# Kernel tuning notes

Measured on AMD Instinct MI355X. Metric: run time of the kernel, lower is better.

The kernel has to match this reference:

```python
import jax, jax.numpy as jnp
import numpy as np


def setup_inputs() -> dict:
    key = jax.random.key(0)
    k1, k2, k3, k4 = jax.random.split(key, 4)
    B, T, M, Din, Dout = 32, 24, 512, 64, 64
    x = jax.random.normal(k1, (B, T, M, Din), dtype=jnp.float32)
    adj = jax.random.uniform(k2, (M, M), dtype=jnp.float32)
    adj = adj / jnp.sum(adj, axis=-1, keepdims=True)  # row-normalized adjacency
    route_weights = jax.random.normal(k3, (M, Din, Dout), dtype=jnp.float32) * 0.05
    route_bias = jax.random.normal(k4, (M, 1, Dout), dtype=jnp.float32) * 0.05
    return {"x": x, "adj": adj, "route_weights": route_weights, "route_bias": route_bias}


def reference(x, adj, route_weights, route_bias):
    B, T, M, _ = x.shape
    xf = x.reshape(B * T, M, -1)                      # [BT, M, Din]
    # shared adjacency applied across all B*T graphs: one contraction instead of
    # a broadcast bmm
    h = jnp.einsum('mn,bnd->bmd', adj, xf)            # [BT, M, Din]
    # per-node (per-route) weight transform + per-route bias
    h = jnp.einsum('bmd,mdl->bml', h, route_weights)  # [BT, M, Dout]
    h = h + route_bias[:, 0, :][None, :, :]           # bias per route m
    return h.reshape(B, T, M, -1)
```

## Files before the change

### kernel.cpp

```cpp
#include <hip/hip_runtime.h>
#include <stdint.h>

typedef short bf16x8 __attribute__((ext_vector_type(8)));
typedef unsigned short u16x8 __attribute__((ext_vector_type(8)));
typedef float f32x4 __attribute__((ext_vector_type(4)));
typedef float f32x8 __attribute__((ext_vector_type(8)));

constexpr int BT_TOT = 768;
constexpr int M_N    = 512;
constexpr int DD     = 64;
constexpr int WROW   = 72;

constexpr size_t ADJ_FRAG_B = (size_t)M_N * M_N * 2;
constexpr size_t XTF_B      = (size_t)BT_TOT * M_N * DD * 2;

__device__ __forceinline__ unsigned short f2bf(float f) {
  unsigned u = __builtin_bit_cast(unsigned, f);
  u += 0x7fffu + ((u >> 16) & 1u);
  return (unsigned short)(u >> 16);
}
__device__ __forceinline__ unsigned pk2(float a, float b) {
  return (unsigned)f2bf(a) | ((unsigned)f2bf(b) << 16);
}


__global__ __launch_bounds__(256)
void prep_adj_frag(const float* __restrict__ adjg, unsigned short* __restrict__ wsadj) {
  int t  = blockIdx.x * 256 + threadIdx.x;
  int m  = t >> 6, ko = t & 63;
  f32x8 a = *(const f32x8*)(adjg + (size_t)m * M_N + ko * 8);
  u16x8 r;
  #pragma unroll
  for (int j = 0; j < 8; ++j) r[j] = f2bf(a[j]);
  size_t g = (size_t)((m >> 4) * 16 + (ko >> 2)) * 64 + (ko & 3) * 16 + (m & 15);
  *(u16x8*)(wsadj + g * 8) = r;
}

__global__ __launch_bounds__(256)
void prep_x_fast(const float* __restrict__ xg, unsigned short* __restrict__ xtf) {
  const int wid = blockIdx.x;
  const int bt  = wid >> 2, q = wid & 3;
  const int tid = threadIdx.x, lane = tid & 63, w = tid >> 6;
  const int gg  = lane >> 4, c4 = lane & 15;

  const float* xb = xg + (size_t)bt * (M_N * DD);
  unsigned short* xo = xtf + (size_t)bt * 32768;

  #pragma unroll
  for (int cc = 0; cc < 2; ++cc) {
    const int c = q * 2 + cc;
    unsigned r0[4], r1[4];
    #pragma unroll
    for (int s2 = 0; s2 < 2; ++s2) {
      #pragma unroll
      for (int sp = 0; sp < 2; ++sp) {
        const int n = c*64 + w*16 + (s2*2 + sp)*4 + gg;
        f32x4 xv = *(const f32x4*)(xb + (size_t)n * DD + c4*4);
        unsigned u0 = pk2(xv.x, xv.y), u1 = pk2(xv.z, xv.w);
        unsigned t0 = __shfl_xor(u0, 32), t1 = __shfl_xor(u1, 32);
        unsigned v0 = (gg & 2) ? t1 : u0, v1 = (gg & 2) ? u1 : t0;
        unsigned s0 = __shfl_xor(v0, 16), s1 = __shfl_xor(v1, 16);
        unsigned F0 = (gg & 1) ? ((s0 >> 16) | (v0 & 0xFFFF0000u))
                               : ((v0 & 0xFFFFu) | (s0 << 16));
        unsigned F1 = (gg & 1) ? ((s1 >> 16) | (v1 & 0xFFFF0000u))
                               : ((v1 & 0xFFFFu) | (s1 << 16));
        if (s2 == 0) { r0[sp*2] = F0; r0[sp*2+1] = F1; }
        else         { r1[sp*2] = F0; r1[sp*2+1] = F1; }
      }
    }
    const int d = c4*4 + gg, dt = d >> 4, l15p = d & 15;
    #pragma unroll
    for (int h = 0; h < 2; ++h) {
      const int o  = w*2 + h;
      const int kl = c*2 + (o >> 2), ggp = o & 3;
      uint4 val;
      if (h == 0) { val.x=r0[0]; val.y=r0[1]; val.z=r0[2]; val.w=r0[3]; }
      else        { val.x=r1[0]; val.y=r1[1]; val.z=r1[2]; val.w=r1[3]; }
      *(uint4*)(xo + ((size_t)(kl*4 + dt)*64 + ggp*16 + l15p) * 8) = val;
    }
  }
}

__global__ __launch_bounds__(256, 3)
void gconv_fast(const unsigned short* __restrict__ adjF,
                const unsigned short* __restrict__ xtf,
                char* __restrict__ dio) {
  __shared__ unsigned short Hb[256 * 72];

  const int wid  = blockIdx.x;
  const int xcd  = wid & 7, slot = wid >> 3;
  const int mb   = slot & 3;
  const int bt0  = ((slot >> 2) * 8 + xcd) * 2;

  const int tid  = threadIdx.x, lane = tid & 63, wv = tid >> 6;
  const int l15  = lane & 15, gg = lane >> 4;

  const unsigned short* xo0 = xtf + (size_t)bt0 * 32768;
  const unsigned short* xo1 = xtf + (size_t)(bt0 + 1) * 32768;

  f32x4 acc[2][2][4];
  #pragma unroll
  for (int bb = 0; bb < 2; ++bb)
    #pragma unroll
    for (int mt = 0; mt < 2; ++mt)
      #pragma unroll
      for (int dt = 0; dt < 4; ++dt) acc[bb][mt][dt] = f32x4{0.f,0.f,0.f,0.f};

  #pragma unroll 4
  for (int kl = 0; kl < 16; ++kl) {
    bf16x8 afr[2];
    #pragma unroll
    for (int mt = 0; mt < 2; ++mt)
      afr[mt] = __builtin_bit_cast(bf16x8, *(const u16x8*)(adjF
          + ((size_t)((mb*8 + wv*2 + mt)*16 + kl)*64 + lane) * 8));
    bf16x8 bfx[2][4];
    #pragma unroll
    for (int dt = 0; dt < 4; ++dt) {
      bfx[0][dt] = __builtin_bit_cast(bf16x8,
          *(const u16x8*)(xo0 + ((size_t)(kl*4 + dt)*64 + lane) * 8));
      bfx[1][dt] = __builtin_bit_cast(bf16x8,
          *(const u16x8*)(xo1 + ((size_t)(kl*4 + dt)*64 + lane) * 8));
    }
    #pragma unroll
    for (int bb = 0; bb < 2; ++bb)
      #pragma unroll
      for (int mt = 0; mt < 2; ++mt)
        #pragma unroll
        for (int dt = 0; dt < 4; ++dt)
          acc[bb][mt][dt] = __builtin_amdgcn_mfma_f32_16x16x32_bf16(
              afr[mt], bfx[bb][dt], acc[bb][mt][dt], 0,0,0);
  }

  #pragma unroll
  for (int bb = 0; bb < 2; ++bb)
    #pragma unroll
    for (int mt = 0; mt < 2; ++mt)
      #pragma unroll
      for (int dt = 0; dt < 4; ++dt)
        #pragma unroll
        for (int r = 0; r < 4; ++r)
          Hb[(bb*128 + wv*32 + mt*16 + gg*4 + r)*72 + dt*16 + l15]
              = f2bf(acc[bb][mt][dt][r]);
  __syncthreads();
  #pragma unroll
  for (int j = 0; j < 8; ++j) {
    const int rl = j*32 + (tid >> 3);
    u16x8 v = *(const u16x8*)(&Hb[rl*72 + (tid & 7)*8]);
    const int bb = rl >> 7, mloc = rl & 127;
    *(u16x8*)(dio + ((size_t)(bt0 + bb)*M_N + mb*128 + mloc)*256 + (tid & 7)*16) = v;
  }
}


__global__ __launch_bounds__(256)
void prep_adj(const float* __restrict__ adjg, unsigned short* __restrict__ wsadj) {
  int i = (blockIdx.x * 256 + threadIdx.x) * 8;
  f32x8 a = *(const f32x8*)(adjg + i);
  u16x8 r;
  #pragma unroll
  for (int j = 0; j < 8; ++j) r[j] = f2bf(a[j]);
  *(u16x8*)(wsadj + i) = r;
}

__global__ __launch_bounds__(256, 4)
void prep_x_fb(const float* __restrict__ xg, char* __restrict__ xout) {
  __shared__ __align__(16) char lds[2][8192];
  const int wid  = blockIdx.x;
  const int bt   = wid >> 1, half = wid & 1;
  const int tid  = threadIdx.x, lane = tid & 63, wv = tid >> 6;
  const int gg   = lane >> 4, c4 = lane & 15;
  const float* xb = xg + (size_t)bt * (M_N * DD);
  f32x4 xv[4];
  auto load_c = [&](int c) {
    #pragma unroll
    for (int s = 0; s < 4; ++s)
      xv[s] = *(const f32x4*)(xb + (size_t)(c*64 + s*16 + wv*4 + gg) * DD + c4*4);
  };
  load_c(half*4);
  #pragma unroll
  for (int cc = 0; cc < 4; ++cc) {
    const int c = half*4 + cc;
    char* xt = &lds[cc & 1][0];
    { const int d = c4*4 + gg, g3d = (d & 7) ^ ((d >> 3) & 7);
      #pragma unroll
      for (int s = 0; s < 4; ++s) {
        const int n4 = s*4 + wv;
        unsigned u0 = pk2(xv[s].x, xv[s].y), u1 = pk2(xv[s].z, xv[s].w);
        unsigned t0 = __shfl_xor(u0, 32), t1 = __shfl_xor(u1, 32);
        unsigned v0 = (gg & 2) ? t1 : u0, v1 = (gg & 2) ? u1 : t0;
        unsigned s0 = __shfl_xor(v0, 16), s1 = __shfl_xor(v1, 16);
        unsigned F0 = (gg & 1) ? ((s0 >> 16) | (v0 & 0xFFFF0000u))
                               : ((v0 & 0xFFFFu) | (s0 << 16));
        unsigned F1 = (gg & 1) ? ((s1 >> 16) | (v1 & 0xFFFF0000u))
                               : ((v1 & 0xFFFFu) | (s1 << 16));
        uint2 o2; o2.x = F0; o2.y = F1;
        *(uint2*)(xt + d*128 + (((n4 >> 1) ^ g3d) * 16) + (n4 & 1)*8) = o2;
      }
    }
    if (cc < 3) load_c(c + 1);
    __syncthreads();
    #pragma unroll
    for (int h = 0; h < 2; ++h) {
      const int g = tid + h*256, d = g >> 3, o = g & 7;
      const int g3d = (d & 7) ^ ((d >> 3) & 7);
      u16x8 val = *(const u16x8*)(xt + d*128 + ((o ^ g3d) * 16));
      *(u16x8*)(xout + ((size_t)(bt*512 + 8*d + c)) * 256 + 128 + o*16) = val;
    }
  }
}

template<bool WS>
__global__ __launch_bounds__(256, 3)
void gconv_fb(const float* __restrict__ adjf,
              const unsigned short* __restrict__ adjb,
              char* __restrict__ dio) {
  const int wid  = blockIdx.x;
  const int xcd  = wid & 7, slot = wid >> 3;
  const int mb   = slot & 3;
  const int bt0  = ((slot >> 2) * 8 + xcd) * 2;
  const int tid  = threadIdx.x, lane = tid & 63, wv = tid >> 6;
  const int l15  = lane & 15, gg = lane >> 4;
  const int mrow = mb*128 + wv*32;
  f32x4 acc[2][2][4];
  #pragma unroll
  for (int bb = 0; bb < 2; ++bb)
    #pragma unroll
    for (int mt = 0; mt < 2; ++mt)
      #pragma unroll
      for (int dt = 0; dt < 4; ++dt) acc[bb][mt][dt] = f32x4{0.f,0.f,0.f,0.f};
  #pragma unroll 4
  for (int kl = 0; kl < 16; ++kl) {
    bf16x8 afr[2];
    #pragma unroll
    for (int mt = 0; mt < 2; ++mt) {
      const int m = mrow + mt*16 + l15;
      if (WS) {
        afr[mt] = __builtin_bit_cast(bf16x8,
            *(const u16x8*)(adjb + (size_t)m*M_N + kl*32 + gg*8));
      } else {
        f32x8 a = *(const f32x8*)(adjf + (size_t)m*M_N + kl*32 + gg*8);
        u16x8 r;
        #pragma unroll
        for (int j = 0; j < 8; ++j) r[j] = f2bf(a[j]);
        afr[mt] = __builtin_bit_cast(bf16x8, r);
      }
    }
    bf16x8 bfx[2][4];
    #pragma unroll
    for (int bb = 0; bb < 2; ++bb)
      #pragma unroll
      for (int dt = 0; dt < 4; ++dt) {
        const int d = dt*16 + l15;
        bfx[bb][dt] = __builtin_bit_cast(bf16x8, *(const u16x8*)(dio
            + ((size_t)((bt0+bb)*512 + 8*d + (kl >> 1))) * 256
            + 128 + (kl & 1)*64 + gg*16));
      }
    #pragma unroll
    for (int bb = 0; bb < 2; ++bb)
      #pragma unroll
      for (int mt = 0; mt < 2; ++mt)
        #pragma unroll
        for (int dt = 0; dt < 4; ++dt)
          acc[bb][mt][dt] = __builtin_amdgcn_mfma_f32_16x16x32_bf16(
              afr[mt], bfx[bb][dt], acc[bb][mt][dt], 0,0,0);
  }
  #pragma unroll
  for (int bb = 0; bb < 2; ++bb)
    #pragma unroll
    for (int mt = 0; mt < 2; ++mt)
      #pragma unroll
      for (int dt = 0; dt < 4; ++dt)
        #pragma unroll
        for (int r = 0; r < 4; ++r) {
          const int m = mrow + mt*16 + gg*4 + r, d = dt*16 + l15;
          *(unsigned short*)(dio + ((size_t)(bt0+bb)*M_N + m)*256 + 2*d)
              = f2bf(acc[bb][mt][dt][r]);
        }
}

__global__ __launch_bounds__(256, 4)
void route_mm(const char* __restrict__ hin,
              const float* __restrict__ wgt,
              const float* __restrict__ bias,
              float* __restrict__ outg) {
  __shared__ unsigned short wb[128 * WROW];
  const int m0    = blockIdx.x * 2;
  const int btblk = blockIdx.y * 64;
  const int tid   = threadIdx.x, lane = tid & 63, wv = tid >> 6;
  const int l15   = lane & 15, gg = lane >> 4;
  const int dp    = tid & 31, lo = tid >> 5;
  { const float* q = wgt + ((size_t)m0*64 + dp*2)*64 + lo*8;
    f32x8 w0 = *(const f32x8*)q;          f32x8 w1 = *(const f32x8*)(q+64);
    f32x8 w2 = *(const f32x8*)(q+4096);   f32x8 w3 = *(const f32x8*)(q+4160);
    #pragma unroll
    for (int e = 0; e < 8; ++e) {
      int lrow = lo*8 + e;
      *(unsigned*)(wb + lrow*WROW + dp*2)        = pk2(w0[e], w1[e]);
      *(unsigned*)(wb + (64 + lrow)*WROW + dp*2) = pk2(w2[e], w3[e]);
    }
  }
  __syncthreads();
  const int btw0 = btblk + wv*16;
  #pragma unroll
  for (int mm = 0; mm < 2; ++mm) {
    const int m = m0 + mm;
    bf16x8 afr[2];
    #pragma unroll
    for (int ks = 0; ks < 2; ++ks) {
      const char* hp = hin + ((size_t)(btw0 + l15)*M_N + m)*256 + ks*64 + gg*16;
      afr[ks] = __builtin_bit_cast(bf16x8, *(const u16x8*)hp);
    }
    f32x4 acc[4];
    #pragma unroll
    for (int lt = 0; lt < 4; ++lt) acc[lt] = f32x4{0.f,0.f,0.f,0.f};
    #pragma unroll
    for (int lt = 0; lt < 4; ++lt)
      #pragma unroll
      for (int ks = 0; ks < 2; ++ks) {
        bf16x8 bfr = __builtin_bit_cast(bf16x8,
            *(const u16x8*)(wb + (mm*64 + lt*16 + l15)*WROW + ks*32 + gg*8));
        acc[lt] = __builtin_amdgcn_mfma_f32_16x16x32_bf16(afr[ks], bfr, acc[lt], 0,0,0);
      }
    #pragma unroll
    for (int lt = 0; lt < 4; ++lt) {
      float bv = bias[m*64 + lt*16 + l15];
      #pragma unroll
      for (int r = 0; r < 4; ++r) {
        size_t row = (size_t)(btw0 + gg*4 + r)*M_N + m;
        outg[row*64 + lt*16 + l15] = acc[lt][r] + bv;
      }
    }
  }
}

extern "C" void kernel_launch(void* const* d_in, const int* in_sizes, int n_in,
                              void* d_out, int out_size, void* d_ws, size_t ws_size,
                              hipStream_t stream) {
  const float* xg   = (const float*)d_in[0];
  const float* adjg = (const float*)d_in[1];
  const float* wgt  = (const float*)d_in[2];
  const float* bg   = (const float*)d_in[3];

  if (ws_size >= ADJ_FRAG_B + XTF_B) {
    unsigned short* adjF = (unsigned short*)d_ws;
    unsigned short* xtf  = (unsigned short*)((char*)d_ws + ADJ_FRAG_B);
    prep_adj_frag<<<dim3(128), dim3(256), 0, stream>>>(adjg, adjF);
    prep_x_fast<<<dim3(BT_TOT * 4), dim3(256), 0, stream>>>(xg, xtf);
    gconv_fast<<<dim3(1536), dim3(256), 0, stream>>>(adjF, xtf, (char*)d_out);
  } else {
    prep_x_fb<<<dim3(BT_TOT * 2), dim3(256), 0, stream>>>(xg, (char*)d_out);
    if (ws_size >= ADJ_FRAG_B) {
      unsigned short* wsadj = (unsigned short*)d_ws;
      prep_adj<<<dim3(M_N * M_N / (256 * 8)), dim3(256), 0, stream>>>(adjg, wsadj);
      gconv_fb<true><<<dim3(1536), dim3(256), 0, stream>>>(adjg, wsadj, (char*)d_out);
    } else {
      gconv_fb<false><<<dim3(1536), dim3(256), 0, stream>>>(adjg, nullptr, (char*)d_out);
    }
  }
  route_mm<<<dim3(M_N/2, BT_TOT/64), dim3(256), 0, stream>>>(
      (const char*)d_out, wgt, bg, (float*)d_out);
}
```

Baseline: 97.89 us.

## Fuse x conversion into graph conv via LDS staging, write compact H workspace

Merges the separate x-to-bf16 fragment prep kernel into the graph-conv kernel. Each 512-thread block converts one bt slice of x into swizzled LDS and computes all 512 rows against the pre-fragmented adjacency. This removes the global round trip of the transformed x. The intermediate H is now written densely to workspace at a 128-byte row stride instead of into the output buffer at a 256-byte stride, so route_mm gains a stride parameter. In exchange, each block reloads all of the adjacency from L2, and the 64KB LDS footprint limits occupancy.

```diff
diff --git a/kernel.cpp b/kernel.cpp
--- a/kernel.cpp
+++ b/kernel.cpp
@@ -12,6 +12,7 @@
 constexpr int WROW   = 72;
 
 constexpr size_t ADJ_FRAG_B = (size_t)M_N * M_N * 2;
+constexpr size_t HWS_B      = (size_t)BT_TOT * M_N * DD * 2;
 constexpr size_t XTF_B      = (size_t)BT_TOT * M_N * DD * 2;
 
 __device__ __forceinline__ unsigned short f2bf(float f) {
@@ -22,7 +23,6 @@
 __device__ __forceinline__ unsigned pk2(float a, float b) {
   return (unsigned)f2bf(a) | ((unsigned)f2bf(b) << 16);
 }
-
 
 __global__ __launch_bounds__(256)
 void prep_adj_frag(const float* __restrict__ adjg, unsigned short* __restrict__ wsadj) {
@@ -36,118 +36,94 @@
   *(u16x8*)(wsadj + g * 8) = r;
 }
 
-__global__ __launch_bounds__(256)
-void prep_x_fast(const float* __restrict__ xg, unsigned short* __restrict__ xtf) {
-  const int wid = blockIdx.x;
-  const int bt  = wid >> 2, q = wid & 3;
-  const int tid = threadIdx.x, lane = tid & 63, w = tid >> 6;
-  const int gg  = lane >> 4, c4 = lane & 15;
+__global__ __launch_bounds__(512, 4)
+void gconv_v12(const float* __restrict__ xg,
+               const unsigned short* __restrict__ adjF,
+               unsigned short* __restrict__ hws) {
+  __shared__ __align__(16) char lds[65536];
+
+  const int bt   = blockIdx.x;
+  const int tid  = threadIdx.x;
+  const int lane = tid & 63;
+  const int w    = tid >> 6;
+  const int l15  = lane & 15;
+  const int gg   = lane >> 4;
+  const int c4   = lane & 15;
 
   const float* xb = xg + (size_t)bt * (M_N * DD);
-  unsigned short* xo = xtf + (size_t)bt * 32768;
-
-  #pragma unroll
-  for (int cc = 0; cc < 2; ++cc) {
-    const int c = q * 2 + cc;
-    unsigned r0[4], r1[4];
-    #pragma unroll
-    for (int s2 = 0; s2 < 2; ++s2) {
-      #pragma unroll
-      for (int sp = 0; sp < 2; ++sp) {
-        const int n = c*64 + w*16 + (s2*2 + sp)*4 + gg;
-        f32x4 xv = *(const f32x4*)(xb + (size_t)n * DD + c4*4);
-        unsigned u0 = pk2(xv.x, xv.y), u1 = pk2(xv.z, xv.w);
-        unsigned t0 = __shfl_xor(u0, 32), t1 = __shfl_xor(u1, 32);
-        unsigned v0 = (gg & 2) ? t1 : u0, v1 = (gg & 2) ? u1 : t0;
-        unsigned s0 = __shfl_xor(v0, 16), s1 = __shfl_xor(v1, 16);
-        unsigned F0 = (gg & 1) ? ((s0 >> 16) | (v0 & 0xFFFF0000u))
-                               : ((v0 & 0xFFFFu) | (s0 << 16));
-        unsigned F1 = (gg & 1) ? ((s1 >> 16) | (v1 & 0xFFFF0000u))
-                               : ((v1 & 0xFFFFu) | (s1 << 16));
-        if (s2 == 0) { r0[sp*2] = F0; r0[sp*2+1] = F1; }
-        else         { r1[sp*2] = F0; r1[sp*2+1] = F1; }
-      }
-    }
-    const int d = c4*4 + gg, dt = d >> 4, l15p = d & 15;
-    #pragma unroll
-    for (int h = 0; h < 2; ++h) {
-      const int o  = w*2 + h;
-      const int kl = c*2 + (o >> 2), ggp = o & 3;
-      uint4 val;
-      if (h == 0) { val.x=r0[0]; val.y=r0[1]; val.z=r0[2]; val.w=r0[3]; }
-      else        { val.x=r1[0]; val.y=r1[1]; val.z=r1[2]; val.w=r1[3]; }
-      *(uint4*)(xo + ((size_t)(kl*4 + dt)*64 + ggp*16 + l15p) * 8) = val;
-    }
-  }
-}
-
-__global__ __launch_bounds__(256, 3)
-void gconv_fast(const unsigned short* __restrict__ adjF,
-                const unsigned short* __restrict__ xtf,
-                char* __restrict__ dio) {
-  __shared__ unsigned short Hb[256 * 72];
-
-  const int wid  = blockIdx.x;
-  const int xcd  = wid & 7, slot = wid >> 3;
-  const int mb   = slot & 3;
-  const int bt0  = ((slot >> 2) * 8 + xcd) * 2;
-
-  const int tid  = threadIdx.x, lane = tid & 63, wv = tid >> 6;
-  const int l15  = lane & 15, gg = lane >> 4;
-
-  const unsigned short* xo0 = xtf + (size_t)bt0 * 32768;
-  const unsigned short* xo1 = xtf + (size_t)(bt0 + 1) * 32768;
-
-  f32x4 acc[2][2][4];
-  #pragma unroll
-  for (int bb = 0; bb < 2; ++bb)
-    #pragma unroll
-    for (int mt = 0; mt < 2; ++mt)
-      #pragma unroll
-      for (int dt = 0; dt < 4; ++dt) acc[bb][mt][dt] = f32x4{0.f,0.f,0.f,0.f};
+
+  #pragma unroll 2
+  for (int c = 0; c < 8; ++c) {
+    unsigned gdw[4];
+    #pragma unroll
+    for (int sp = 0; sp < 2; ++sp) {
+      const int n = c*64 + w*8 + sp*4 + gg;
+      f32x4 xv = *(const f32x4*)(xb + (size_t)n * DD + c4*4);
+      unsigned u0 = pk2(xv.x, xv.y), u1 = pk2(xv.z, xv.w);
+      unsigned t0 = __shfl_xor(u0, 32), t1 = __shfl_xor(u1, 32);
+      unsigned v0 = (gg & 2) ? t1 : u0, v1 = (gg & 2) ? u1 : t0;
+      unsigned s0 = __shfl_xor(v0, 16), s1 = __shfl_xor(v1, 16);
+      unsigned F0 = (gg & 1) ? ((s0 >> 16) | (v0 & 0xFFFF0000u))
+                             : ((v0 & 0xFFFFu) | (s0 << 16));
+      unsigned F1 = (gg & 1) ? ((s1 >> 16) | (v1 & 0xFFFF0000u))
+                             : ((v1 & 0xFFFFu) | (s1 << 16));
+      gdw[sp*2] = F0; gdw[sp*2+1] = F1;
+    }
+    const int d  = c4*4 + gg;
+    const int dt = d >> 4;
+    const int o  = c*8 + w;
+    uint4 val; val.x = gdw[0]; val.y = gdw[1]; val.z = gdw[2]; val.w = gdw[3];
+    *(uint4*)(lds + ((((o >> 2)*4 + dt)*64 + (o & 3)*16 + ((d & 15) ^ dt)) << 4)) = val;
+  }
+  __syncthreads();
+
+  f32x4 acc[4][4];
+  #pragma unroll
+  for (int mt = 0; mt < 4; ++mt)
+    #pragma unroll
+    for (int dt = 0; dt < 4; ++dt) acc[mt][dt] = f32x4{0.f,0.f,0.f,0.f};
 
   #pragma unroll 4
   for (int kl = 0; kl < 16; ++kl) {
-    bf16x8 afr[2];
-    #pragma unroll
-    for (int mt = 0; mt < 2; ++mt)
+    bf16x8 afr[4];
+    #pragma unroll
+    for (int mt = 0; mt < 4; ++mt)
       afr[mt] = __builtin_bit_cast(bf16x8, *(const u16x8*)(adjF
-          + ((size_t)((mb*8 + wv*2 + mt)*16 + kl)*64 + lane) * 8));
-    bf16x8 bfx[2][4];
-    #pragma unroll
-    for (int dt = 0; dt < 4; ++dt) {
-      bfx[0][dt] = __builtin_bit_cast(bf16x8,
-          *(const u16x8*)(xo0 + ((size_t)(kl*4 + dt)*64 + lane) * 8));
-      bfx[1][dt] = __builtin_bit_cast(bf16x8,
-          *(const u16x8*)(xo1 + ((size_t)(kl*4 + dt)*64 + lane) * 8));
-    }
-    #pragma unroll
-    for (int bb = 0; bb < 2; ++bb)
-      #pragma unroll
-      for (int mt = 0; mt < 2; ++mt)
-        #pragma unroll
-        for (int dt = 0; dt < 4; ++dt)
-          acc[bb][mt][dt] = __builtin_amdgcn_mfma_f32_16x16x32_bf16(
-              afr[mt], bfx[bb][dt], acc[bb][mt][dt], 0,0,0);
-  }
-
-  #pragma unroll
-  for (int bb = 0; bb < 2; ++bb)
-    #pragma unroll
-    for (int mt = 0; mt < 2; ++mt)
+          + ((size_t)((w*4 + mt)*16 + kl)*64 + lane) * 8));
+    bf16x8 bfx[4];
+    #pragma unroll
+    for (int dt = 0; dt < 4; ++dt)
+      bfx[dt] = __builtin_bit_cast(bf16x8, *(const u16x8*)(lds
+          + (((kl*4 + dt)*64 + gg*16 + (l15 ^ dt)) << 4)));
+    #pragma unroll
+    for (int mt = 0; mt < 4; ++mt)
       #pragma unroll
       for (int dt = 0; dt < 4; ++dt)
-        #pragma unroll
-        for (int r = 0; r < 4; ++r)
-          Hb[(bb*128 + wv*32 + mt*16 + gg*4 + r)*72 + dt*16 + l15]
-              = f2bf(acc[bb][mt][dt][r]);
+        acc[mt][dt] = __builtin_amdgcn_mfma_f32_16x16x32_bf16(
+            afr[mt], bfx[dt], acc[mt][dt], 0,0,0);
+  }
+
   __syncthreads();
   #pragma unroll
-  for (int j = 0; j < 8; ++j) {
-    const int rl = j*32 + (tid >> 3);
-    u16x8 v = *(const u16x8*)(&Hb[rl*72 + (tid & 7)*8]);
-    const int bb = rl >> 7, mloc = rl & 127;
-    *(u16x8*)(dio + ((size_t)(bt0 + bb)*M_N + mb*128 + mloc)*256 + (tid & 7)*16) = v;
+  for (int mt = 0; mt < 4; ++mt)
+    #pragma unroll
+    for (int dt = 0; dt < 4; ++dt)
+      #pragma unroll
+      for (int r = 0; r < 4; ++r) {
+        const int m = w*64 + mt*16 + gg*4 + r;
+        const int d = dt*16 + l15;
+        const int q = d >> 3;
+        *(unsigned short*)(lds + m*128 + (((q ^ (m & 7)) << 4)) + (d & 7)*2)
+            = f2bf(acc[mt][dt][r]);
+      }
+  __syncthreads();
+  char* hrow = (char*)(hws + (size_t)bt * (M_N * DD));
+  #pragma unroll
+  for (int i = 0; i < 8; ++i) {
+    const int g = tid + i*512;
+    const int m = g >> 3, q = g & 7;
+    uint4 v = *(const uint4*)(lds + m*128 + ((q ^ (m & 7)) << 4));
+    *(uint4*)(hrow + g*16) = v;
   }
 }
 
@@ -279,7 +255,7 @@
 }
 
 __global__ __launch_bounds__(256, 4)
-void route_mm(const char* __restrict__ hin,
+void route_mm(const char* __restrict__ hin, int hstride,
               const float* __restrict__ wgt,
               const float* __restrict__ bias,
               float* __restrict__ outg) {
@@ -307,7 +283,7 @@
     bf16x8 afr[2];
     #pragma unroll
     for (int ks = 0; ks < 2; ++ks) {
-      const char* hp = hin + ((size_t)(btw0 + l15)*M_N + m)*256 + ks*64 + gg*16;
+      const char* hp = hin + ((size_t)(btw0 + l15)*M_N + m)*hstride + ks*64 + gg*16;
       afr[ks] = __builtin_bit_cast(bf16x8, *(const u16x8*)hp);
     }
     f32x4 acc[4];
@@ -341,12 +317,13 @@
   const float* wgt  = (const float*)d_in[2];
   const float* bg   = (const float*)d_in[3];
 
-  if (ws_size >= ADJ_FRAG_B + XTF_B) {
+  if (ws_size >= ADJ_FRAG_B + HWS_B) {
     unsigned short* adjF = (unsigned short*)d_ws;
-    unsigned short* xtf  = (unsigned short*)((char*)d_ws + ADJ_FRAG_B);
+    unsigned short* hws  = (unsigned short*)((char*)d_ws + ADJ_FRAG_B);
     prep_adj_frag<<<dim3(128), dim3(256), 0, stream>>>(adjg, adjF);
-    prep_x_fast<<<dim3(BT_TOT * 4), dim3(256), 0, stream>>>(xg, xtf);
-    gconv_fast<<<dim3(1536), dim3(256), 0, stream>>>(adjF, xtf, (char*)d_out);
+    gconv_v12<<<dim3(BT_TOT), dim3(512), 0, stream>>>(xg, adjF, hws);
+    route_mm<<<dim3(M_N/2, BT_TOT/64), dim3(256), 0, stream>>>(
+        (const char*)hws, 128, wgt, bg, (float*)d_out);
   } else {
     prep_x_fb<<<dim3(BT_TOT * 2), dim3(256), 0, stream>>>(xg, (char*)d_out);
     if (ws_size >= ADJ_FRAG_B) {
@@ -356,7 +333,7 @@
     } else {
       gconv_fb<false><<<dim3(1536), dim3(256), 0, stream>>>(adjg, nullptr, (char*)d_out);
     }
-  }
-  route_mm<<<dim3(M_N/2, BT_TOT/64), dim3(256), 0, stream>>>(
-      (const char*)d_out, wgt, bg, (float*)d_out);
-}
+    route_mm<<<dim3(M_N/2, BT_TOT/64), dim3(256), 0, stream>>>(
+        (const char*)d_out, 256, wgt, bg, (float*)d_out);
+  }
+}
```

Result: no change. 96.90 us (-1.0%).

## Double-buffer x tiles via global_load_lds and store H in route-major workspace layout

Applied to the files above, without the earlier changes.

The graph-conv kernel now stages x fragments into double-buffered LDS with async global_load_lds, prefetching the next K chunk while MFMAs run on the current one, with one barrier per chunk. The intermediate H moves out of the output buffer into a separate workspace laid out as [m][ks][bt][32], so route_mm reads contiguous 16-row blocks per route instead of strided rows. The fast path now needs extra workspace, so a smaller workspace falls back to the old path. This adds LDS use and barriers per block.

```diff
diff --git a/kernel.cpp b/kernel.cpp
--- a/kernel.cpp
+++ b/kernel.cpp
@@ -13,6 +13,7 @@
 
 constexpr size_t ADJ_FRAG_B = (size_t)M_N * M_N * 2;
 constexpr size_t XTF_B      = (size_t)BT_TOT * M_N * DD * 2;
+constexpr size_t HWS_B      = (size_t)BT_TOT * M_N * DD * 2;
 
 __device__ __forceinline__ unsigned short f2bf(float f) {
   unsigned u = __builtin_bit_cast(unsigned, f);
@@ -22,7 +23,11 @@
 __device__ __forceinline__ unsigned pk2(float a, float b) {
   return (unsigned)f2bf(a) | ((unsigned)f2bf(b) << 16);
 }
-
+__device__ __forceinline__ void gload16(const unsigned short* g, char* l) {
+  __builtin_amdgcn_global_load_lds(
+      (const __attribute__((address_space(1))) unsigned int*)g,
+      (__attribute__((address_space(3))) unsigned int*)l, 16, 0, 0);
+}
 
 __global__ __launch_bounds__(256)
 void prep_adj_frag(const float* __restrict__ adjg, unsigned short* __restrict__ wsadj) {
@@ -82,10 +87,10 @@
 }
 
 __global__ __launch_bounds__(256, 3)
-void gconv_fast(const unsigned short* __restrict__ adjF,
-                const unsigned short* __restrict__ xtf,
-                char* __restrict__ dio) {
-  __shared__ unsigned short Hb[256 * 72];
+void gconv_r13(const unsigned short* __restrict__ adjF,
+               const unsigned short* __restrict__ xtf,
+               unsigned short* __restrict__ h2) {
+  __shared__ __align__(16) char lds[36864];
 
   const int wid  = blockIdx.x;
   const int xcd  = wid & 7, slot = wid >> 3;
@@ -95,8 +100,17 @@
   const int tid  = threadIdx.x, lane = tid & 63, wv = tid >> 6;
   const int l15  = lane & 15, gg = lane >> 4;
 
-  const unsigned short* xo0 = xtf + (size_t)bt0 * 32768;
-  const unsigned short* xo1 = xtf + (size_t)(bt0 + 1) * 32768;
+  auto stage = [&](int c) {
+    char* buf = lds + (c & 1) * 16384;
+    #pragma unroll
+    for (int j = 0; j < 4; ++j) {
+      const int su = j*4 + wv;
+      const int bb = su >> 3, kk = (su >> 2) & 1, dt = su & 3;
+      const unsigned short* src = xtf + (size_t)(bt0 + bb) * 32768
+                                + ((size_t)((2*c + kk)*4 + dt)*64 + lane) * 8;
+      gload16(src, buf + su*1024 + lane*16);
+    }
+  };
 
   f32x4 acc[2][2][4];
   #pragma unroll
@@ -106,48 +120,63 @@
       #pragma unroll
       for (int dt = 0; dt < 4; ++dt) acc[bb][mt][dt] = f32x4{0.f,0.f,0.f,0.f};
 
-  #pragma unroll 4
-  for (int kl = 0; kl < 16; ++kl) {
-    bf16x8 afr[2];
+  stage(0);
+  __syncthreads();
+
+  #pragma unroll 1
+  for (int c = 0; c < 8; ++c) {
+    bf16x8 afr[2][2];
+    #pragma unroll
+    for (int kk = 0; kk < 2; ++kk)
+      #pragma unroll
+      for (int mt = 0; mt < 2; ++mt)
+        afr[kk][mt] = __builtin_bit_cast(bf16x8, *(const u16x8*)(adjF
+            + ((size_t)((mb*8 + wv*2 + mt)*16 + (2*c + kk))*64 + lane) * 8));
+    if (c < 7) stage(c + 1);
+
+    const char* buf = lds + (c & 1) * 16384;
+    #pragma unroll
+    for (int kk = 0; kk < 2; ++kk) {
+      bf16x8 bfx[2][4];
+      #pragma unroll
+      for (int bb = 0; bb < 2; ++bb)
+        #pragma unroll
+        for (int dt = 0; dt < 4; ++dt)
+          bfx[bb][dt] = __builtin_bit_cast(bf16x8,
+              *(const u16x8*)(buf + ((bb*2 + kk)*4 + dt)*1024 + lane*16));
+      #pragma unroll
+      for (int bb = 0; bb < 2; ++bb)
+        #pragma unroll
+        for (int mt = 0; mt < 2; ++mt)
+          #pragma unroll
+          for (int dt = 0; dt < 4; ++dt)
+            acc[bb][mt][dt] = __builtin_amdgcn_mfma_f32_16x16x32_bf16(
+                afr[kk][mt], bfx[bb][dt], acc[bb][mt][dt], 0,0,0);
+    }
+    __syncthreads();
+  }
+
+  unsigned short* hl = (unsigned short*)lds;
+  #pragma unroll
+  for (int bb = 0; bb < 2; ++bb)
     #pragma unroll
     for (int mt = 0; mt < 2; ++mt)
-      afr[mt] = __builtin_bit_cast(bf16x8, *(const u16x8*)(adjF
-          + ((size_t)((mb*8 + wv*2 + mt)*16 + kl)*64 + lane) * 8));
-    bf16x8 bfx[2][4];
-    #pragma unroll
-    for (int dt = 0; dt < 4; ++dt) {
-      bfx[0][dt] = __builtin_bit_cast(bf16x8,
-          *(const u16x8*)(xo0 + ((size_t)(kl*4 + dt)*64 + lane) * 8));
-      bfx[1][dt] = __builtin_bit_cast(bf16x8,
-          *(const u16x8*)(xo1 + ((size_t)(kl*4 + dt)*64 + lane) * 8));
-    }
-    #pragma unroll
-    for (int bb = 0; bb < 2; ++bb)
-      #pragma unroll
-      for (int mt = 0; mt < 2; ++mt)
-        #pragma unroll
-        for (int dt = 0; dt < 4; ++dt)
-          acc[bb][mt][dt] = __builtin_amdgcn_mfma_f32_16x16x32_bf16(
-              afr[mt], bfx[bb][dt], acc[bb][mt][dt], 0,0,0);
-  }
-
-  #pragma unroll
-  for (int bb = 0; bb < 2; ++bb)
-    #pragma unroll
-    for (int mt = 0; mt < 2; ++mt)
       #pragma unroll
       for (int dt = 0; dt < 4; ++dt)
         #pragma unroll
-        for (int r = 0; r < 4; ++r)
-          Hb[(bb*128 + wv*32 + mt*16 + gg*4 + r)*72 + dt*16 + l15]
-              = f2bf(acc[bb][mt][dt][r]);
+        for (int r = 0; r < 4; ++r) {
+          const int rl = bb*128 + wv*32 + mt*16 + gg*4 + r;
+          hl[rl*72 + dt*16 + l15] = f2bf(acc[bb][mt][dt][r]);
+        }
   __syncthreads();
   #pragma unroll
-  for (int j = 0; j < 8; ++j) {
-    const int rl = j*32 + (tid >> 3);
-    u16x8 v = *(const u16x8*)(&Hb[rl*72 + (tid & 7)*8]);
+  for (int i = 0; i < 8; ++i) {
+    const int g  = tid + i*256;
+    const int rl = g >> 3, qq = g & 7;
+    u16x8 v = *(const u16x8*)(hl + rl*72 + qq*8);
     const int bb = rl >> 7, mloc = rl & 127;
-    *(u16x8*)(dio + ((size_t)(bt0 + bb)*M_N + mb*128 + mloc)*256 + (tid & 7)*16) = v;
+    const int m  = mb*128 + mloc, ks = qq >> 2, o = qq & 3;
+    *(u16x8*)((char*)h2 + (((size_t)m*2 + ks)*768 + bt0 + bb)*64 + o*16) = v;
   }
 }
 
@@ -278,6 +307,7 @@
         }
 }
 
+template<bool H2L>
 __global__ __launch_bounds__(256, 4)
 void route_mm(const char* __restrict__ hin,
               const float* __restrict__ wgt,
@@ -307,7 +337,9 @@
     bf16x8 afr[2];
     #pragma unroll
     for (int ks = 0; ks < 2; ++ks) {
-      const char* hp = hin + ((size_t)(btw0 + l15)*M_N + m)*256 + ks*64 + gg*16;
+      const char* hp = H2L
+        ? hin + (((size_t)m*2 + ks)*768 + btw0 + l15)*64 + gg*16
+        : hin + ((size_t)(btw0 + l15)*M_N + m)*256 + ks*64 + gg*16;
       afr[ks] = __builtin_bit_cast(bf16x8, *(const u16x8*)hp);
     }
     f32x4 acc[4];
@@ -341,12 +373,15 @@
   const float* wgt  = (const float*)d_in[2];
   const float* bg   = (const float*)d_in[3];
 
-  if (ws_size >= ADJ_FRAG_B + XTF_B) {
+  if (ws_size >= ADJ_FRAG_B + XTF_B + HWS_B) {
     unsigned short* adjF = (unsigned short*)d_ws;
     unsigned short* xtf  = (unsigned short*)((char*)d_ws + ADJ_FRAG_B);
+    unsigned short* h2   = (unsigned short*)((char*)d_ws + ADJ_FRAG_B + XTF_B);
     prep_adj_frag<<<dim3(128), dim3(256), 0, stream>>>(adjg, adjF);
     prep_x_fast<<<dim3(BT_TOT * 4), dim3(256), 0, stream>>>(xg, xtf);
-    gconv_fast<<<dim3(1536), dim3(256), 0, stream>>>(adjF, xtf, (char*)d_out);
+    gconv_r13<<<dim3(1536), dim3(256), 0, stream>>>(adjF, xtf, h2);
+    route_mm<true><<<dim3(M_N/2, BT_TOT/64), dim3(256), 0, stream>>>(
+        (const char*)h2, wgt, bg, (float*)d_out);
   } else {
     prep_x_fb<<<dim3(BT_TOT * 2), dim3(256), 0, stream>>>(xg, (char*)d_out);
     if (ws_size >= ADJ_FRAG_B) {
@@ -356,7 +391,7 @@
     } else {
       gconv_fb<false><<<dim3(1536), dim3(256), 0, stream>>>(adjg, nullptr, (char*)d_out);
     }
-  }
-  route_mm<<<dim3(M_N/2, BT_TOT/64), dim3(256), 0, stream>>>(
-      (const char*)d_out, wgt, bg, (float*)d_out);
-}
+    route_mm<false><<<dim3(M_N/2, BT_TOT/64), dim3(256), 0, stream>>>(
+        (const char*)d_out, wgt, bg, (float*)d_out);
+  }
+}
```

Result: slower. 101.9 us (+4.1%).
